# Kernel tuning notes

Measured on AMD Instinct MI355X. Metric: run time of the kernel, lower is better.

## Reference

```python
import jax, jax.numpy as jnp
import numpy as np

B = 8          # batch (number of ragged segments)
N = 4096       # trigram sets per sequence (uniform segments)
K = 3          # trigram token ids per set
V = 100000     # vocab_size
H = 1024       # hidden_size
SEQ = 2048     # sequence_length / seq_len


def setup_inputs() -> dict:
    key = jax.random.key(0)
    k1, k2 = jax.random.split(key)
    trigram_token_ids = jax.random.randint(k1, (B * N, K), 0, V, dtype=jnp.int32)
    # each position covered by exactly 2 trigram sets; per-segment positions start at 0
    pos_one = (jnp.arange(N, dtype=jnp.int32) // 2)  # [N], values 0..SEQ-1
    trigram_set_position_ids = jnp.tile(pos_one, B)  # [B*N]
    starts = jnp.arange(B, dtype=jnp.int32) * N
    trigram_token_ids_offsets = jnp.stack([starts, starts + N], axis=1)  # [B,2]
    std = (2.0 / (5.0 * H)) ** 0.5  # pythia init
    W = jax.random.normal(k2, (V, H), dtype=jnp.float32) * std
    return {
        "trigram_set_position_ids": trigram_set_position_ids,
        "trigram_token_ids": trigram_token_ids,
        "trigram_token_ids_offsets": trigram_token_ids_offsets,
        "seq_len": SEQ,
        "W": W,
    }


def reference(trigram_set_position_ids, trigram_token_ids, trigram_token_ids_offsets, seq_len, W):
    # Uniform ragged segments: reshape flat arrays to [B, n, ...] using offsets count.
    b = trigram_token_ids_offsets.shape[0]
    total, k = trigram_token_ids.shape
    n = total // b
    tok = trigram_token_ids.reshape(b, n, k)          # [B, n, K]
    pos = trigram_set_position_ids.reshape(b, n)      # [B, n]
    # gather + mean-aggregate over the K trigram ids of each set
    emb = W[tok].mean(axis=2)                         # [B, n, H]

    def scatter_one(p, e):
        # index_add scatter of set embeddings onto sequence positions
        s = jax.ops.segment_sum(e, p, num_segments=seq_len)                       # [seq, H]
        c = jax.ops.segment_sum(jnp.ones((n,), e.dtype), p, num_segments=seq_len)  # [seq]
        c = jnp.where(c == 0, jnp.ones((), e.dtype), c)  # counts of 0 -> 1 (normalization guard)
        return s / c[:, None]

    return jax.vmap(scatter_one)(pos, emb)            # [B, seq, H]
```

## Files before the change

### kernel.cpp

```cpp
#include <hip/hip_runtime.h>

#define CAP 8
#define MAXK 8

__global__ void build_map_kernel(const int* __restrict__ pos_ids,
                                 const int* __restrict__ tok,
                                 int total, int n_per, int seq, int K,
                                 int* __restrict__ counts,
                                 int* __restrict__ toktab) {
    int i = blockIdx.x * blockDim.x + threadIdx.x;
    if (i >= total) return;
    int b = i / n_per;
    int p = pos_ids[i];
    if ((unsigned)p >= (unsigned)seq) return;
    int bp = b * seq + p;
    int c = atomicAdd(&counts[bp], 1);
    if (c < CAP) {
        int* dst = toktab + (size_t)bp * (CAP * K) + c * K;
        for (int k = 0; k < K; ++k) dst[k] = tok[i * K + k];
    }
}

#define SORT2(a, b) { int _lo = min(a, b); int _hi = max(a, b); a = _lo; b = _hi; }

__global__ void gather_out_kernel(const float* __restrict__ W,
                                  const int* __restrict__ counts,
                                  const int* __restrict__ toktab,
                                  float* __restrict__ out,
                                  int K, int H) {
    int bp = blockIdx.x;
    int cnt = counts[bp];
    int ce = cnt < CAP ? cnt : CAP;
    int ntok = ce * K;
    const int* tp = toktab + (size_t)bp * (CAP * K);
    int h = threadIdx.x * 4;

    float4 acc = make_float4(0.f, 0.f, 0.f, 0.f);

    if (ntok == 6) {
        int t0 = tp[0], t1 = tp[1], t2 = tp[2], t3 = tp[3], t4 = tp[4], t5 = tp[5];
        SORT2(t1, t2) SORT2(t4, t5) SORT2(t0, t2) SORT2(t3, t5)
        SORT2(t0, t1) SORT2(t3, t4) SORT2(t1, t4) SORT2(t0, t3)
        SORT2(t2, t5) SORT2(t1, t3) SORT2(t2, t4) SORT2(t2, t3)
        const float4 v0 = *(const float4*)(W + (size_t)t0 * H + h);
        const float4 v1 = *(const float4*)(W + (size_t)t1 * H + h);
        const float4 v2 = *(const float4*)(W + (size_t)t2 * H + h);
        const float4 v3 = *(const float4*)(W + (size_t)t3 * H + h);
        const float4 v4 = *(const float4*)(W + (size_t)t4 * H + h);
        const float4 v5 = *(const float4*)(W + (size_t)t5 * H + h);
        acc.x = ((v0.x + v1.x) + (v2.x + v3.x)) + (v4.x + v5.x);
        acc.y = ((v0.y + v1.y) + (v2.y + v3.y)) + (v4.y + v5.y);
        acc.z = ((v0.z + v1.z) + (v2.z + v3.z)) + (v4.z + v5.z);
        acc.w = ((v0.w + v1.w) + (v2.w + v3.w)) + (v4.w + v5.w);
    } else if (ntok > 0) {
        __shared__ int s_tok[CAP * MAXK];
        if (threadIdx.x == 0) {
            for (int j = 0; j < ntok; ++j) s_tok[j] = tp[j];
            for (int a = 1; a < ntok; ++a) {
                int v = s_tok[a];
                int q = a - 1;
                while (q >= 0 && s_tok[q] > v) { s_tok[q + 1] = s_tok[q]; --q; }
                s_tok[q + 1] = v;
            }
        }
        __syncthreads();
        for (int j = 0; j < ntok; ++j) {
            int t = s_tok[j];
            const float4 v = *(const float4*)(W + (size_t)t * H + h);
            acc.x += v.x; acc.y += v.y; acc.z += v.z; acc.w += v.w;
        }
    }

    float denom = (float)K * (float)(cnt > 0 ? cnt : 1);
    float scale = 1.0f / denom;
    acc.x *= scale; acc.y *= scale; acc.z *= scale; acc.w *= scale;
    *(float4*)(out + (size_t)bp * H + h) = acc;
}

extern "C" void kernel_launch(void* const* d_in, const int* in_sizes, int n_in,
                              void* d_out, int out_size, void* d_ws, size_t ws_size,
                              hipStream_t stream) {
    const int*   pos_ids = (const int*)d_in[0];
    const int*   tok     = (const int*)d_in[1];
    const float* W       = (const float*)d_in[4];
    float*       out     = (float*)d_out;

    const int B     = in_sizes[2] / 2;
    const int total = in_sizes[0];
    const int n_per = total / B;
    const int K     = in_sizes[1] / total;
    const int H     = 1024;
    const int seq   = out_size / (B * H);

    int* counts = (int*)d_ws;
    int* toktab = counts + (size_t)B * seq;

    hipMemsetAsync(counts, 0, (size_t)B * seq * sizeof(int), stream);

    int bthreads = 256;
    int bblocks  = (total + bthreads - 1) / bthreads;
    build_map_kernel<<<bblocks, bthreads, 0, stream>>>(pos_ids, tok, total,
                                                       n_per, seq, K,
                                                       counts, toktab);

    gather_out_kernel<<<B * seq, H / 4, 0, stream>>>(W, counts, toktab,
                                                     out, K, H);
}
```

Before: 83.72 us.

## Sort token rows in separate kernel and process 16 rows per gather block

Token-id sorting moves out of the gather kernel into its own small kernel that sorts each row's ids in place. The gather kernel now handles 16 output rows per block, with 16 float4 accumulators per thread, which gives many independent W loads in flight per thread. Output is written with nontemporal stores. The cost is an extra kernel launch and higher register pressure, and there are 16x fewer blocks, which may reduce occupancy.

```diff
diff --git a/kernel.cpp b/kernel.cpp
--- a/kernel.cpp
+++ b/kernel.cpp
@@ -1,7 +1,7 @@
 #include <hip/hip_runtime.h>
 
 #define CAP 8
-#define MAXK 8
+#define RPB 16
 
 __global__ void build_map_kernel(const int* __restrict__ pos_ids,
                                  const int* __restrict__ tok,
@@ -23,58 +23,96 @@
 
 #define SORT2(a, b) { int _lo = min(a, b); int _hi = max(a, b); a = _lo; b = _hi; }
 
-__global__ void gather_out_kernel(const float* __restrict__ W,
-                                  const int* __restrict__ counts,
-                                  const int* __restrict__ toktab,
-                                  float* __restrict__ out,
-                                  int K, int H) {
-    int bp = blockIdx.x;
-    int cnt = counts[bp];
+__global__ void sort_rows_kernel(const int* __restrict__ counts,
+                                 int* __restrict__ toktab,
+                                 int nrows, int K) {
+    int i = blockIdx.x * blockDim.x + threadIdx.x;
+    if (i >= nrows) return;
+    int cnt = counts[i];
     int ce = cnt < CAP ? cnt : CAP;
-    int ntok = ce * K;
-    const int* tp = toktab + (size_t)bp * (CAP * K);
+    int n = ce * K;
+    int stride = CAP * K;
+    int* row = toktab + (size_t)i * stride;
+    if (n == 6) {
+        int t0=row[0],t1=row[1],t2=row[2],t3=row[3],t4=row[4],t5=row[5];
+        SORT2(t1,t2) SORT2(t4,t5) SORT2(t0,t2) SORT2(t3,t5)
+        SORT2(t0,t1) SORT2(t3,t4) SORT2(t1,t4) SORT2(t0,t3)
+        SORT2(t2,t5) SORT2(t1,t3) SORT2(t2,t4) SORT2(t2,t3)
+        row[0]=t0;row[1]=t1;row[2]=t2;row[3]=t3;row[4]=t4;row[5]=t5;
+    } else if (n > 1) {
+        int tmp[CAP * 8];
+        if (n > CAP * 8) n = CAP * 8;
+        for (int j = 0; j < n; ++j) tmp[j] = row[j];
+        for (int a = 1; a < n; ++a) {
+            int v = tmp[a]; int q = a - 1;
+            while (q >= 0 && tmp[q] > v) { tmp[q + 1] = tmp[q]; --q; }
+            tmp[q + 1] = v;
+        }
+        for (int j = 0; j < n; ++j) row[j] = tmp[j];
+    }
+}
+
+__global__ __launch_bounds__(256, 4)
+void gather_out_kernel(const float* __restrict__ W,
+                       const int* __restrict__ counts,
+                       const int* __restrict__ toktab,
+                       float* __restrict__ out,
+                       int K, int H, int nrows) {
+    int r0 = blockIdx.x * RPB;
     int h = threadIdx.x * 4;
+    int stride = CAP * K;
 
-    float4 acc = make_float4(0.f, 0.f, 0.f, 0.f);
+    int cnt[RPB];
+    bool allsix = true;
+    #pragma unroll
+    for (int r = 0; r < RPB; ++r) {
+        int row = r0 + r;
+        cnt[r] = (row < nrows) ? counts[row] : 0;
+        int ce = cnt[r] < CAP ? cnt[r] : CAP;
+        if (ce * K != 6) allsix = false;
+    }
 
-    if (ntok == 6) {
-        int t0 = tp[0], t1 = tp[1], t2 = tp[2], t3 = tp[3], t4 = tp[4], t5 = tp[5];
-        SORT2(t1, t2) SORT2(t4, t5) SORT2(t0, t2) SORT2(t3, t5)
-        SORT2(t0, t1) SORT2(t3, t4) SORT2(t1, t4) SORT2(t0, t3)
-        SORT2(t2, t5) SORT2(t1, t3) SORT2(t2, t4) SORT2(t2, t3)
-        const float4 v0 = *(const float4*)(W + (size_t)t0 * H + h);
-        const float4 v1 = *(const float4*)(W + (size_t)t1 * H + h);
-        const float4 v2 = *(const float4*)(W + (size_t)t2 * H + h);
-        const float4 v3 = *(const float4*)(W + (size_t)t3 * H + h);
-        const float4 v4 = *(const float4*)(W + (size_t)t4 * H + h);
-        const float4 v5 = *(const float4*)(W + (size_t)t5 * H + h);
-        acc.x = ((v0.x + v1.x) + (v2.x + v3.x)) + (v4.x + v5.x);
-        acc.y = ((v0.y + v1.y) + (v2.y + v3.y)) + (v4.y + v5.y);
-        acc.z = ((v0.z + v1.z) + (v2.z + v3.z)) + (v4.z + v5.z);
-        acc.w = ((v0.w + v1.w) + (v2.w + v3.w)) + (v4.w + v5.w);
-    } else if (ntok > 0) {
-        __shared__ int s_tok[CAP * MAXK];
-        if (threadIdx.x == 0) {
-            for (int j = 0; j < ntok; ++j) s_tok[j] = tp[j];
-            for (int a = 1; a < ntok; ++a) {
-                int v = s_tok[a];
-                int q = a - 1;
-                while (q >= 0 && s_tok[q] > v) { s_tok[q + 1] = s_tok[q]; --q; }
-                s_tok[q + 1] = v;
+    float4 acc[RPB];
+    #pragma unroll
+    for (int r = 0; r < RPB; ++r) acc[r] = make_float4(0.f, 0.f, 0.f, 0.f);
+
+    if (allsix) {
+        #pragma unroll
+        for (int j = 0; j < 6; ++j) {
+            #pragma unroll
+            for (int r = 0; r < RPB; ++r) {
+                int t = toktab[(size_t)(r0 + r) * stride + j];
+                const float4 v = *(const float4*)(W + (size_t)t * H + h);
+                acc[r].x += v.x; acc[r].y += v.y;
+                acc[r].z += v.z; acc[r].w += v.w;
             }
         }
-        __syncthreads();
-        for (int j = 0; j < ntok; ++j) {
-            int t = s_tok[j];
-            const float4 v = *(const float4*)(W + (size_t)t * H + h);
-            acc.x += v.x; acc.y += v.y; acc.z += v.z; acc.w += v.w;
+    } else {
+        #pragma unroll
+        for (int r = 0; r < RPB; ++r) {
+            int ce = cnt[r] < CAP ? cnt[r] : CAP;
+            int ntok = ce * K;
+            for (int j = 0; j < ntok; ++j) {
+                int t = toktab[(size_t)(r0 + r) * stride + j];
+                const float4 v = *(const float4*)(W + (size_t)t * H + h);
+                acc[r].x += v.x; acc[r].y += v.y;
+                acc[r].z += v.z; acc[r].w += v.w;
+            }
         }
     }
 
-    float denom = (float)K * (float)(cnt > 0 ? cnt : 1);
-    float scale = 1.0f / denom;
-    acc.x *= scale; acc.y *= scale; acc.z *= scale; acc.w *= scale;
-    *(float4*)(out + (size_t)bp * H + h) = acc;
+    #pragma unroll
+    for (int r = 0; r < RPB; ++r) {
+        int row = r0 + r;
+        if (row >= nrows) continue;
+        float denom = (float)K * (float)(cnt[r] > 0 ? cnt[r] : 1);
+        float s = 1.0f / denom;
+        float* op = out + (size_t)row * H + h;
+        __builtin_nontemporal_store(acc[r].x * s, op + 0);
+        __builtin_nontemporal_store(acc[r].y * s, op + 1);
+        __builtin_nontemporal_store(acc[r].z * s, op + 2);
+        __builtin_nontemporal_store(acc[r].w * s, op + 3);
+    }
 }
 
 extern "C" void kernel_launch(void* const* d_in, const int* in_sizes, int n_in,
@@ -91,11 +129,12 @@
     const int K     = in_sizes[1] / total;
     const int H     = 1024;
     const int seq   = out_size / (B * H);
+    const int nrows = B * seq;
 
     int* counts = (int*)d_ws;
-    int* toktab = counts + (size_t)B * seq;
+    int* toktab = counts + (size_t)nrows;
 
-    hipMemsetAsync(counts, 0, (size_t)B * seq * sizeof(int), stream);
+    hipMemsetAsync(counts, 0, (size_t)nrows * sizeof(int), stream);
 
     int bthreads = 256;
     int bblocks  = (total + bthreads - 1) / bthreads;
@@ -103,6 +142,11 @@
                                                        n_per, seq, K,
                                                        counts, toktab);
 
-    gather_out_kernel<<<B * seq, H / 4, 0, stream>>>(W, counts, toktab,
-                                                     out, K, H);
+    int sblocks = (nrows + bthreads - 1) / bthreads;
+    sort_rows_kernel<<<sblocks, bthreads, 0, stream>>>(counts, toktab,
+                                                       nrows, K);
+
+    int gblocks = (nrows + RPB - 1) / RPB;
+    gather_out_kernel<<<gblocks, H / 4, 0, stream>>>(W, counts, toktab,
+                                                     out, K, H, nrows);
 }
```

After: 88.82 us. 6.1% more time.
